# Optimization experiments

Measured on AMD Instinct MI355X. Metric: run time of the kernel, lower is better.

Reference implementation:

```python
import jax, jax.numpy as jnp
import numpy as np

LR = 0.1          # RMSprop learning rate (set_hyper_parameters)
ALPHA = 0.9       # RMSprop decay
ITERATIONS = 5    # SVGD iterations
INV_SIG2 = 1.0    # Gaussian posterior score scale (concrete post_grad)
EPS = 1e-8


def setup_inputs() -> dict:
    key = jax.random.key(0)
    k1, k2 = jax.random.split(key)
    x = jax.random.normal(k1, (8, 2048, 8), dtype=jnp.float32)          # [B, N, D] particles
    observation = jax.random.normal(k2, (8, 8), dtype=jnp.float32)      # [B, D]
    return {"x": x, "observation": observation}


def _svgd(x, observation):
    B, N, D = x.shape
    # median heuristic bandwidth h = median(pairwise dist)^2 / log(N), per batch, no-grad
    sq = jnp.sum((x[:, :, None, :] - x[:, None, :, :]) ** 2, axis=-1)   # [B, N, N]
    med = jnp.median(jnp.sqrt(sq).reshape(B, -1), axis=-1)              # [B]
    h = jax.lax.stop_gradient(med ** 2 / jnp.log(jnp.float32(N)))       # [B]
    inv_N = jnp.float32(1.0 / N)

    def post_grad(xc):
        # Gaussian posterior score: d/dx log N(x; observation, sigma^2 I)
        return (observation[:, None, :] - xc) * INV_SIG2                # [B, N, D]

    def step(carry, _):
        xc, s = carry
        dist = xc[:, :, None, :] - xc[:, None, :, :]                    # [B, i, j, D]
        K = jnp.exp(-jnp.sum(dist ** 2, axis=-1) / h[:, None, None])    # [B, i, j] rbf
        g = post_grad(xc)                                               # [B, j, D]
        # phi_i = (1/N) sum_j [ K_ij * g_j + (2/h)(x_i - x_j) K_ij ]
        phi = inv_N * (jnp.einsum('bij,bjd->bid', K, g)
                       + (2.0 / h)[:, None, None] * jnp.einsum('bij,bijd->bid', K, dist))
        # RMSprop (state update under no_grad in the original)
        s = jax.lax.stop_gradient(ALPHA * s + (1.0 - ALPHA) * phi ** 2)
        xc = xc + LR * phi / (jnp.sqrt(s) + EPS)
        return (xc, s), None

    (x, _), _ = jax.lax.scan(step, (x, jnp.zeros_like(x)), None, length=ITERATIONS)
    return x


def reference(x, observation):
    return _svgd(x, observation)
```

## Files before the change

kernel.cpp:

```cpp
#include <hip/hip_runtime.h>
#include <cstdint>

#define BATCH 8
#define NPART 2048
#define DDIM 8
#define NN (NPART * NPART)

#define MJCHUNK 128
#define SJCHUNK 512

constexpr float LR = 0.1f;
constexpr float ALPHA = 0.9f;
constexpr float EPS = 1e-8f;
constexpr float INV_N = 1.0f / (float)NPART;
constexpr float LOG2E = 1.44269504088896340736f;

typedef float v2f __attribute__((ext_vector_type(2)));
typedef float v4f __attribute__((ext_vector_type(4)));

__global__ __launch_bounds__(256) void init_ws_k(unsigned* __restrict__ hist,
                                                 unsigned* __restrict__ prefix,
                                                 unsigned* __restrict__ rank) {
    const int tid = blockIdx.x * 256 + threadIdx.x;
    if (tid < BATCH * 2 * 256) hist[tid] = 0u;
    if (tid < BATCH * 2) {
        prefix[tid] = 0u;
        rank[tid] = (unsigned)(NN / 2) + (unsigned)(tid & 1);
    }
}

__global__ __launch_bounds__(256) void median_hist_k(const float* __restrict__ x,
                                                     unsigned* __restrict__ hist,
                                                     const unsigned* __restrict__ prefix,
                                                     int shift) {
    __shared__ __align__(16) v4f xs0[MJCHUNK];
    __shared__ __align__(16) v4f xs1[MJCHUNK];
    __shared__ float rs[MJCHUNK];
    __shared__ unsigned lh[256 * 32];

    const int b = blockIdx.x;
    const int tid = threadIdx.x;
    const int lane = tid & 63;
    const int slot = tid & 31;
    const int trow = tid >> 6;
    const float* xb = x + (size_t)b * NPART * DDIM;

    const unsigned p0 = prefix[2 * b + 0];
    const unsigned p1 = prefix[2 * b + 1];
    const bool same = (p0 == p1);
    const unsigned mask = (shift == 24) ? 0u : (0xFFFFFFFFu << (shift + 8));

    const int ibase = blockIdx.y * 16 + trow * 4;
    v2f xi[4][4];
    float q[4];
#pragma unroll
    for (int rr = 0; rr < 4; ++rr) {
        const v4f t0 = ((const v4f*)(xb + (size_t)(ibase + rr) * DDIM))[0];
        const v4f t1 = ((const v4f*)(xb + (size_t)(ibase + rr) * DDIM))[1];
        xi[rr][0] = t0.xy; xi[rr][1] = t0.zw;
        xi[rr][2] = t1.xy; xi[rr][3] = t1.zw;
        q[rr] = t0.x * t0.x + t0.y * t0.y + t0.z * t0.z + t0.w * t0.w
              + t1.x * t1.x + t1.y * t1.y + t1.z * t1.z + t1.w * t1.w;
    }

    const int nsel = same ? 1 : 2;
    for (int sel = 0; sel < nsel; ++sel) {
        const unsigned pref = sel ? p1 : p0;
        __syncthreads();
        for (int t = tid; t < 256 * 32; t += 256) lh[t] = 0u;

        for (int cbase = 0; cbase < NPART; cbase += MJCHUNK) {
            __syncthreads();
            for (int t = tid; t < MJCHUNK; t += 256) {
                const v4f u0 = ((const v4f*)(xb + (size_t)(cbase + t) * DDIM))[0];
                const v4f u1 = ((const v4f*)(xb + (size_t)(cbase + t) * DDIM))[1];
                xs0[t] = u0;
                xs1[t] = u1;
                rs[t] = u0.x * u0.x + u0.y * u0.y + u0.z * u0.z + u0.w * u0.w
                      + u1.x * u1.x + u1.y * u1.y + u1.z * u1.z + u1.w * u1.w;
            }
            __syncthreads();
#pragma unroll
            for (int j = lane; j < MJCHUNK; j += 64) {
                const v4f A = xs0[j];
                const v4f B = xs1[j];
                const float r = rs[j];
                const v2f A0 = A.xy, A1 = A.zw, B0 = B.xy, B1 = B.zw;
#pragma unroll
                for (int rr = 0; rr < 4; ++rr) {
                    v2f p = A0 * xi[rr][0];
                    p += A1 * xi[rr][1];
                    p += B0 * xi[rr][2];
                    p += B1 * xi[rr][3];
                    const float sq = fmaxf(fmaf(-2.0f, p.x + p.y, q[rr] + r), 0.0f);
                    const unsigned u = __float_as_uint(sq);
                    if ((u & mask) == pref)
                        atomicAdd(&lh[((u >> shift) & 255u) * 32 + slot], 1u);
                }
            }
        }
        __syncthreads();
        unsigned tot = 0;
#pragma unroll
        for (int sct = 0; sct < 32; ++sct) tot += lh[tid * 32 + ((sct + tid) & 31)];
        if (tot) {
            atomicAdd(&hist[b * 512 + sel * 256 + tid], tot);
            if (same) atomicAdd(&hist[b * 512 + 256 + tid], tot);
        }
    }
}

__global__ void median_scan_k(unsigned* __restrict__ hist,
                              unsigned* __restrict__ prefix,
                              unsigned* __restrict__ rank,
                              int shift,
                              float* __restrict__ hpar) {
    __shared__ unsigned selv[16];
    const int t = threadIdx.x;
    if (t < 16) {
        const unsigned r = rank[t];
        const unsigned* hb = hist + t * 256;
        unsigned cum = 0;
        int bin = 0;
        for (; bin < 256; ++bin) {
            const unsigned c = hb[bin];
            if (cum + c >= r) break;
            cum += c;
        }
        if (bin > 255) bin = 255;
        const unsigned np = prefix[t] | ((unsigned)bin << shift);
        prefix[t] = np;
        rank[t] = r - cum;
        selv[t] = np;
    }
    __syncthreads();
    for (int q = t; q < 16 * 256; q += 64) hist[q] = 0u;
    if (shift == 8 && t < BATCH) {
        const float v1 = __uint_as_float(selv[2 * t + 0]);
        const float v2 = __uint_as_float(selv[2 * t + 1]);
        const float med = 0.5f * (sqrtf(v1) + sqrtf(v2));
        const float h = (med * med) / logf((float)NPART);
        hpar[2 * t + 0] = -LOG2E / h;
        hpar[2 * t + 1] = 2.0f / h;
    }
}

__global__ __launch_bounds__(256, 4) void svgd_step_k(const float* __restrict__ x_in,
                                                      float* __restrict__ x_out,
                                                      float* __restrict__ s,
                                                      const float* __restrict__ hpar,
                                                      const float* __restrict__ obs,
                                                      int first) {
    __shared__ __align__(16) float smem[4608];
    v4f* xs0 = (v4f*)smem;
    v4f* xs1 = (v4f*)(smem + 2048);
    float* rs = smem + 4096;
    float (*part)[8][9] = (float (*)[8][9])smem;

    const int b = blockIdx.x;
    const int tid = threadIdx.x;
    const int lane = tid & 63;
    const int trow = tid >> 6;
    const float* xb = x_in + (size_t)b * NPART * DDIM;

    const float nih2 = hpar[2 * b + 0];
    const float c2 = hpar[2 * b + 1];
    const float cdot2 = -2.0f * nih2;

    const int ibase = blockIdx.y * 16 + trow * 4;
    v2f xi[4][4];
    float q[4];
#pragma unroll
    for (int rr = 0; rr < 4; ++rr) {
        const v4f t0 = ((const v4f*)(xb + (size_t)(ibase + rr) * DDIM))[0];
        const v4f t1 = ((const v4f*)(xb + (size_t)(ibase + rr) * DDIM))[1];
        xi[rr][0] = t0.xy; xi[rr][1] = t0.zw;
        xi[rr][2] = t1.xy; xi[rr][3] = t1.zw;
        q[rr] = nih2 * (t0.x * t0.x + t0.y * t0.y + t0.z * t0.z + t0.w * t0.w
                      + t1.x * t1.x + t1.y * t1.y + t1.z * t1.z + t1.w * t1.w);
    }

    float S0[4] = {0, 0, 0, 0};
    v2f V[4][4];
#pragma unroll
    for (int rr = 0; rr < 4; ++rr)
#pragma unroll
        for (int k = 0; k < 4; ++k) V[rr][k] = (v2f){0, 0};

    for (int cbase = 0; cbase < NPART; cbase += SJCHUNK) {
        __syncthreads();
        for (int t = tid; t < SJCHUNK; t += 256) {
            const v4f u0 = ((const v4f*)(xb + (size_t)(cbase + t) * DDIM))[0];
            const v4f u1 = ((const v4f*)(xb + (size_t)(cbase + t) * DDIM))[1];
            xs0[t] = u0;
            xs1[t] = u1;
            rs[t] = nih2 * (u0.x * u0.x + u0.y * u0.y + u0.z * u0.z + u0.w * u0.w
                          + u1.x * u1.x + u1.y * u1.y + u1.z * u1.z + u1.w * u1.w);
        }
        __syncthreads();
#pragma unroll 2
        for (int j = lane; j < SJCHUNK; j += 64) {
            const v4f A = xs0[j];
            const v4f B = xs1[j];
            const float r = rs[j];
            const v2f A0 = A.xy, A1 = A.zw, B0 = B.xy, B1 = B.zw;
#pragma unroll
            for (int rr = 0; rr < 4; ++rr) {
                v2f p = A0 * xi[rr][0];
                p += A1 * xi[rr][1];
                p += B0 * xi[rr][2];
                p += B1 * xi[rr][3];
                const float K = __builtin_amdgcn_exp2f(fmaf(cdot2, p.x + p.y, q[rr] + r));
                S0[rr] += K;
                const v2f K2 = {K, K};
                V[rr][0] += A0 * K2;
                V[rr][1] += A1 * K2;
                V[rr][2] += B0 * K2;
                V[rr][3] += B1 * K2;
            }
        }
    }

    __syncthreads();
#pragma unroll
    for (int rr = 0; rr < 4; ++rr) {
        float t0 = S0[rr];
        float t1 = V[rr][0].x, t2 = V[rr][0].y;
        float t3 = V[rr][1].x, t4 = V[rr][1].y;
        float t5 = V[rr][2].x, t6 = V[rr][2].y;
        float t7 = V[rr][3].x, t8 = V[rr][3].y;
        t0 += __shfl_xor(t0, 32); t0 += __shfl_xor(t0, 16); t0 += __shfl_xor(t0, 8);
        t1 += __shfl_xor(t1, 32); t1 += __shfl_xor(t1, 16); t1 += __shfl_xor(t1, 8);
        t2 += __shfl_xor(t2, 32); t2 += __shfl_xor(t2, 16); t2 += __shfl_xor(t2, 8);
        t3 += __shfl_xor(t3, 32); t3 += __shfl_xor(t3, 16); t3 += __shfl_xor(t3, 8);
        t4 += __shfl_xor(t4, 32); t4 += __shfl_xor(t4, 16); t4 += __shfl_xor(t4, 8);
        t5 += __shfl_xor(t5, 32); t5 += __shfl_xor(t5, 16); t5 += __shfl_xor(t5, 8);
        t6 += __shfl_xor(t6, 32); t6 += __shfl_xor(t6, 16); t6 += __shfl_xor(t6, 8);
        t7 += __shfl_xor(t7, 32); t7 += __shfl_xor(t7, 16); t7 += __shfl_xor(t7, 8);
        t8 += __shfl_xor(t8, 32); t8 += __shfl_xor(t8, 16); t8 += __shfl_xor(t8, 8);
        if (lane < 8) {
            const int row = trow * 4 + rr;
            part[row][lane][0] = t0;
            part[row][lane][1] = t1;
            part[row][lane][2] = t2;
            part[row][lane][3] = t3;
            part[row][lane][4] = t4;
            part[row][lane][5] = t5;
            part[row][lane][6] = t6;
            part[row][lane][7] = t7;
            part[row][lane][8] = t8;
        }
    }
    __syncthreads();

    if (tid < 128) {
        const int d2i = tid & 7;
        const int r2 = tid >> 3;
        const int i2 = blockIdx.y * 16 + r2;
        float S0t = 0.0f, Vt = 0.0f;
#pragma unroll
        for (int l = 0; l < 8; ++l) {
            S0t += part[r2][l][0];
            Vt += part[r2][l][1 + d2i];
        }
        const size_t idx = ((size_t)b * NPART + i2) * DDIM + d2i;
        const float xid = x_in[idx];
        const float obsd = obs[b * DDIM + d2i];
        const float U = fmaf(S0t, xid, -Vt);
        const float T = fmaf(S0t, obsd - xid, U);
        const float phi = INV_N * fmaf(c2, U, T);
        float sv;
        if (first) {
            sv = (1.0f - ALPHA) * phi * phi;
        } else {
            sv = ALPHA * s[idx] + (1.0f - ALPHA) * phi * phi;
        }
        s[idx] = sv;
        x_out[idx] = xid + LR * phi / (sqrtf(sv) + EPS);
    }
}

extern "C" void kernel_launch(void* const* d_in, const int* in_sizes, int n_in,
                              void* d_out, int out_size, void* d_ws, size_t ws_size,
                              hipStream_t stream) {
    const float* x0 = (const float*)d_in[0];
    const float* obs = (const float*)d_in[1];
    float* out = (float*)d_out;

    float* xa = (float*)d_ws;
    float* s = xa + BATCH * NPART * DDIM;
    unsigned* hist = (unsigned*)(s + BATCH * NPART * DDIM);
    unsigned* prefix = hist + BATCH * 2 * 256;
    unsigned* rank = prefix + BATCH * 2;
    float* hpar = (float*)(rank + BATCH * 2);

    init_ws_k<<<16, 256, 0, stream>>>(hist, prefix, rank);

    for (int r = 0; r < 3; ++r) {
        const int shift = 24 - 8 * r;
        median_hist_k<<<dim3(BATCH, 128), 256, 0, stream>>>(x0, hist, prefix, shift);
        median_scan_k<<<1, 64, 0, stream>>>(hist, prefix, rank, shift, hpar);
    }

    svgd_step_k<<<dim3(BATCH, 128), 256, 0, stream>>>(x0, out, s, hpar, obs, 1);
    svgd_step_k<<<dim3(BATCH, 128), 256, 0, stream>>>(out, xa, s, hpar, obs, 0);
    svgd_step_k<<<dim3(BATCH, 128), 256, 0, stream>>>(xa, out, s, hpar, obs, 0);
    svgd_step_k<<<dim3(BATCH, 128), 256, 0, stream>>>(out, xa, s, hpar, obs, 0);
    svgd_step_k<<<dim3(BATCH, 128), 256, 0, stream>>>(xa, out, s, hpar, obs, 0);
}
```

Before: 227.4 us.

## Exploit distance symmetry in median histogram and fold scan into last block

The median radix-select histogram now counts only the upper triangle of the pairwise distance matrix, weighting each pair by 2 and adding the N zero diagonal entries separately. This halves the distance work. Each block handles a strip and its mirror strip so the triangular load stays balanced across half as many blocks. The separate scan kernel is removed: the last block to finish, detected with an atomic done counter, performs the bin selection, which saves three launches. The cost is extra atomics, threadfence ordering, and reliance on the last-block pattern being correct.

```diff
diff --git a/kernel.cpp b/kernel.cpp
--- a/kernel.cpp
+++ b/kernel.cpp
@@ -8,6 +8,7 @@
 
 #define MJCHUNK 128
 #define SJCHUNK 512
+#define HBLOCKS (BATCH * 64)
 
 constexpr float LR = 0.1f;
 constexpr float ALPHA = 0.9f;
@@ -20,23 +21,30 @@
 
 __global__ __launch_bounds__(256) void init_ws_k(unsigned* __restrict__ hist,
                                                  unsigned* __restrict__ prefix,
-                                                 unsigned* __restrict__ rank) {
+                                                 unsigned* __restrict__ rank,
+                                                 unsigned* __restrict__ done) {
     const int tid = blockIdx.x * 256 + threadIdx.x;
     if (tid < BATCH * 2 * 256) hist[tid] = 0u;
     if (tid < BATCH * 2) {
         prefix[tid] = 0u;
         rank[tid] = (unsigned)(NN / 2) + (unsigned)(tid & 1);
     }
+    if (tid == 0) *done = 0u;
 }
 
 __global__ __launch_bounds__(256) void median_hist_k(const float* __restrict__ x,
                                                      unsigned* __restrict__ hist,
-                                                     const unsigned* __restrict__ prefix,
+                                                     unsigned* __restrict__ prefix,
+                                                     unsigned* __restrict__ rank,
+                                                     float* __restrict__ hpar,
+                                                     unsigned* __restrict__ done,
                                                      int shift) {
     __shared__ __align__(16) v4f xs0[MJCHUNK];
     __shared__ __align__(16) v4f xs1[MJCHUNK];
     __shared__ float rs[MJCHUNK];
     __shared__ unsigned lh[256 * 32];
+    __shared__ unsigned selv[16];
+    __shared__ unsigned s_islast;
 
     const int b = blockIdx.x;
     const int tid = threadIdx.x;
@@ -50,52 +58,56 @@
     const bool same = (p0 == p1);
     const unsigned mask = (shift == 24) ? 0u : (0xFFFFFFFFu << (shift + 8));
 
-    const int ibase = blockIdx.y * 16 + trow * 4;
-    v2f xi[4][4];
-    float q[4];
-#pragma unroll
-    for (int rr = 0; rr < 4; ++rr) {
-        const v4f t0 = ((const v4f*)(xb + (size_t)(ibase + rr) * DDIM))[0];
-        const v4f t1 = ((const v4f*)(xb + (size_t)(ibase + rr) * DDIM))[1];
-        xi[rr][0] = t0.xy; xi[rr][1] = t0.zw;
-        xi[rr][2] = t1.xy; xi[rr][3] = t1.zw;
-        q[rr] = t0.x * t0.x + t0.y * t0.y + t0.z * t0.z + t0.w * t0.w
-              + t1.x * t1.x + t1.y * t1.y + t1.z * t1.z + t1.w * t1.w;
-    }
-
     const int nsel = same ? 1 : 2;
     for (int sel = 0; sel < nsel; ++sel) {
         const unsigned pref = sel ? p1 : p0;
         __syncthreads();
         for (int t = tid; t < 256 * 32; t += 256) lh[t] = 0u;
 
-        for (int cbase = 0; cbase < NPART; cbase += MJCHUNK) {
-            __syncthreads();
-            for (int t = tid; t < MJCHUNK; t += 256) {
-                const v4f u0 = ((const v4f*)(xb + (size_t)(cbase + t) * DDIM))[0];
-                const v4f u1 = ((const v4f*)(xb + (size_t)(cbase + t) * DDIM))[1];
-                xs0[t] = u0;
-                xs1[t] = u1;
-                rs[t] = u0.x * u0.x + u0.y * u0.y + u0.z * u0.z + u0.w * u0.w
-                      + u1.x * u1.x + u1.y * u1.y + u1.z * u1.z + u1.w * u1.w;
+        for (int sp = 0; sp < 2; ++sp) {
+            const int strip = sp ? (127 - (int)blockIdx.y) : (int)blockIdx.y;
+            const int ibase = strip * 16 + trow * 4;
+            v2f xi[4][4];
+            float q[4];
+#pragma unroll
+            for (int rr = 0; rr < 4; ++rr) {
+                const v4f t0 = ((const v4f*)(xb + (size_t)(ibase + rr) * DDIM))[0];
+                const v4f t1 = ((const v4f*)(xb + (size_t)(ibase + rr) * DDIM))[1];
+                xi[rr][0] = t0.xy; xi[rr][1] = t0.zw;
+                xi[rr][2] = t1.xy; xi[rr][3] = t1.zw;
+                q[rr] = t0.x * t0.x + t0.y * t0.y + t0.z * t0.z + t0.w * t0.w
+                      + t1.x * t1.x + t1.y * t1.y + t1.z * t1.z + t1.w * t1.w;
             }
-            __syncthreads();
-#pragma unroll
-            for (int j = lane; j < MJCHUNK; j += 64) {
-                const v4f A = xs0[j];
-                const v4f B = xs1[j];
-                const float r = rs[j];
-                const v2f A0 = A.xy, A1 = A.zw, B0 = B.xy, B1 = B.zw;
-#pragma unroll
-                for (int rr = 0; rr < 4; ++rr) {
-                    v2f p = A0 * xi[rr][0];
-                    p += A1 * xi[rr][1];
-                    p += B0 * xi[rr][2];
-                    p += B1 * xi[rr][3];
-                    const float sq = fmaxf(fmaf(-2.0f, p.x + p.y, q[rr] + r), 0.0f);
-                    const unsigned u = __float_as_uint(sq);
-                    if ((u & mask) == pref)
-                        atomicAdd(&lh[((u >> shift) & 255u) * 32 + slot], 1u);
+            const int c0 = (strip >> 3) << 7;
+            for (int cbase = c0; cbase < NPART; cbase += MJCHUNK) {
+                __syncthreads();
+                for (int t = tid; t < MJCHUNK; t += 256) {
+                    const v4f u0 = ((const v4f*)(xb + (size_t)(cbase + t) * DDIM))[0];
+                    const v4f u1 = ((const v4f*)(xb + (size_t)(cbase + t) * DDIM))[1];
+                    xs0[t] = u0;
+                    xs1[t] = u1;
+                    rs[t] = u0.x * u0.x + u0.y * u0.y + u0.z * u0.z + u0.w * u0.w
+                          + u1.x * u1.x + u1.y * u1.y + u1.z * u1.z + u1.w * u1.w;
+                }
+                __syncthreads();
+#pragma unroll
+                for (int j = lane; j < MJCHUNK; j += 64) {
+                    const int jg = cbase + j;
+                    const v4f A = xs0[j];
+                    const v4f B = xs1[j];
+                    const float r = rs[j];
+                    const v2f A0 = A.xy, A1 = A.zw, B0 = B.xy, B1 = B.zw;
+#pragma unroll
+                    for (int rr = 0; rr < 4; ++rr) {
+                        v2f p = A0 * xi[rr][0];
+                        p += A1 * xi[rr][1];
+                        p += B0 * xi[rr][2];
+                        p += B1 * xi[rr][3];
+                        const float sq = fmaxf(fmaf(-2.0f, p.x + p.y, q[rr] + r), 0.0f);
+                        const unsigned u = __float_as_uint(sq);
+                        if (jg > ibase + rr && (u & mask) == pref)
+                            atomicAdd(&lh[((u >> shift) & 255u) * 32 + slot], 2u);
+                    }
                 }
             }
         }
@@ -108,40 +120,45 @@
             if (same) atomicAdd(&hist[b * 512 + 256 + tid], tot);
         }
     }
-}
-
-__global__ void median_scan_k(unsigned* __restrict__ hist,
-                              unsigned* __restrict__ prefix,
-                              unsigned* __restrict__ rank,
-                              int shift,
-                              float* __restrict__ hpar) {
-    __shared__ unsigned selv[16];
-    const int t = threadIdx.x;
-    if (t < 16) {
-        const unsigned r = rank[t];
-        const unsigned* hb = hist + t * 256;
-        unsigned cum = 0;
-        int bin = 0;
-        for (; bin < 256; ++bin) {
-            const unsigned c = hb[bin];
-            if (cum + c >= r) break;
-            cum += c;
-        }
-        if (bin > 255) bin = 255;
-        const unsigned np = prefix[t] | ((unsigned)bin << shift);
-        prefix[t] = np;
-        rank[t] = r - cum;
-        selv[t] = np;
-    }
+
     __syncthreads();
-    for (int q = t; q < 16 * 256; q += 64) hist[q] = 0u;
-    if (shift == 8 && t < BATCH) {
-        const float v1 = __uint_as_float(selv[2 * t + 0]);
-        const float v2 = __uint_as_float(selv[2 * t + 1]);
-        const float med = 0.5f * (sqrtf(v1) + sqrtf(v2));
-        const float h = (med * med) / logf((float)NPART);
-        hpar[2 * t + 0] = -LOG2E / h;
-        hpar[2 * t + 1] = 2.0f / h;
+    if (tid == 0) {
+        __threadfence();
+        s_islast = (atomicAdd(done, 1u) == (unsigned)(HBLOCKS - 1)) ? 1u : 0u;
+    }
+    __syncthreads();
+    if (s_islast) {
+        __threadfence();
+        if (tid < 16) {
+            const unsigned prefT = prefix[tid];
+            unsigned* hb = hist + tid * 256;
+            if ((0u & mask) == prefT) atomicAdd(&hb[0], (unsigned)NPART);
+            const unsigned r = rank[tid];
+            unsigned cum = 0;
+            int bin = 0;
+            for (; bin < 256; ++bin) {
+                const unsigned c = atomicAdd(&hb[bin], 0u);
+                if (cum + c >= r) break;
+                cum += c;
+            }
+            if (bin > 255) bin = 255;
+            const unsigned np = prefT | ((unsigned)bin << shift);
+            prefix[tid] = np;
+            rank[tid] = r - cum;
+            selv[tid] = np;
+        }
+        __syncthreads();
+        for (int qq = tid; qq < 16 * 256; qq += 256) hist[qq] = 0u;
+        if (shift == 8 && tid < BATCH) {
+            const float v1 = __uint_as_float(selv[2 * tid + 0]);
+            const float v2 = __uint_as_float(selv[2 * tid + 1]);
+            const float med = 0.5f * (sqrtf(v1) + sqrtf(v2));
+            const float h = (med * med) / logf((float)NPART);
+            hpar[2 * tid + 0] = -LOG2E / h;
+            hpar[2 * tid + 1] = 2.0f / h;
+        }
+        __syncthreads();
+        if (tid == 0) *done = 0u;
     }
 }
 
@@ -293,14 +310,13 @@
     unsigned* prefix = hist + BATCH * 2 * 256;
     unsigned* rank = prefix + BATCH * 2;
     float* hpar = (float*)(rank + BATCH * 2);
-
-    init_ws_k<<<16, 256, 0, stream>>>(hist, prefix, rank);
-
-    for (int r = 0; r < 3; ++r) {
-        const int shift = 24 - 8 * r;
-        median_hist_k<<<dim3(BATCH, 128), 256, 0, stream>>>(x0, hist, prefix, shift);
-        median_scan_k<<<1, 64, 0, stream>>>(hist, prefix, rank, shift, hpar);
-    }
+    unsigned* done = (unsigned*)(hpar + BATCH * 2);
+
+    init_ws_k<<<16, 256, 0, stream>>>(hist, prefix, rank, done);
+
+    median_hist_k<<<dim3(BATCH, 64), 256, 0, stream>>>(x0, hist, prefix, rank, hpar, done, 24);
+    median_hist_k<<<dim3(BATCH, 64), 256, 0, stream>>>(x0, hist, prefix, rank, hpar, done, 16);
+    median_hist_k<<<dim3(BATCH, 64), 256, 0, stream>>>(x0, hist, prefix, rank, hpar, done, 8);
 
     svgd_step_k<<<dim3(BATCH, 128), 256, 0, stream>>>(x0, out, s, hpar, obs, 1);
     svgd_step_k<<<dim3(BATCH, 128), 256, 0, stream>>>(out, xa, s, hpar, obs, 0);
```

Result: slower. 253.5 us (+11.5%).
